# Kernel optimization log

Hardware: AMD Instinct MI355X
Metric: run time of the kernel (lower is better)

## Reference

```python
import jax, jax.numpy as jnp
import numpy as np

N_TOKEN = 50000
D_EMBED = 512
D_PROJ = 1024
CUTOFFS = [10000, 30000, 50000]  # cutoffs + [n_token]
N_CLUSTERS = len(CUTOFFS) - 1    # 2


def setup_inputs() -> dict:
    key = jax.random.key(0)
    ks = jax.random.split(key, 8)
    s = 0.02
    return {
        "hidden": jax.random.normal(ks[0], (4096, D_PROJ), jnp.float32),
        "target": jax.random.randint(ks[1], (4096,), 0, N_TOKEN, jnp.int64),
        # div_val == 1: one big output embedding, sliced per cluster
        "weight": jax.random.normal(ks[2], (N_TOKEN, D_EMBED), jnp.float32) * s,
        "bias": jnp.zeros((N_TOKEN,), jnp.float32),
        "cluster_weight": jax.random.normal(ks[3], (N_CLUSTERS, D_EMBED), jnp.float32) * s,
        "cluster_bias": jnp.zeros((N_CLUSTERS,), jnp.float32),
        # one [d_proj, d_embed] projection per cluster (head + 2 tails)
        "projs": jax.random.normal(ks[4], (N_CLUSTERS + 1, D_PROJ, D_EMBED), jnp.float32) * s,
    }


def _adaptive_logprob(hidden, target, weight, bias, cluster_weight, cluster_bias, projs):
    c0 = CUTOFFS[0]
    n = hidden.shape[0]
    # head: first-cluster vocab + one logit per tail cluster
    head_w = jnp.concatenate([weight[:c0], cluster_weight], axis=0)      # [c0+K, d_embed]
    head_b = jnp.concatenate([bias[:c0], cluster_bias], axis=0)          # [c0+K]
    h0 = hidden @ projs[0]                                               # [N, d_embed]
    head_lp = jax.nn.log_softmax(h0 @ head_w.T + head_b, axis=-1)        # [N, c0+K]

    # tokens in head cluster
    head_idx = jnp.clip(target, 0, c0 - 1)
    lp = jnp.take_along_axis(head_lp, head_idx[:, None], axis=1)[:, 0]
    out = jnp.where(target < c0, lp, 0.0)

    # tail clusters
    for i in range(1, N_CLUSTERS + 1):
        l, r = CUTOFFS[i - 1], CUTOFFS[i]
        hi = hidden @ projs[i]                                           # [N, d_embed]
        tail_lp = jax.nn.log_softmax(hi @ weight[l:r].T + bias[l:r], axis=-1)  # [N, r-l]
        t_idx = jnp.clip(target - l, 0, r - l - 1)
        tlp = jnp.take_along_axis(tail_lp, t_idx[:, None], axis=1)[:, 0]
        lp_i = head_lp[:, c0 + i - 1] + tlp
        out = jnp.where((target >= l) & (target < r), lp_i, out)

    return -out  # nll per token, [N]


def reference(hidden, target, weight, bias, cluster_weight, cluster_bias, projs):
    tgt_len = target.shape[0]
    nll = _adaptive_logprob(hidden[-tgt_len:], target, weight, bias,
                            cluster_weight, cluster_bias, projs)
    return nll.reshape(tgt_len, -1)  # [N, 1], matches loss.view(tgt_len, -1)
```

## Files before the change

kernel.cpp:

```cpp
#include <hip/hip_runtime.h>
#include <math.h>

#define NT 4096
#define DP 1024
#define DE 512
#define C0 10000
#define CUT1 30000
#define TAILV 20000
#define WROWS 50112
#define NBH 79
#define NBT 157

typedef unsigned short ushort_t;
typedef short bf8 __attribute__((ext_vector_type(8)));
typedef float f4 __attribute__((ext_vector_type(4)));

__device__ __forceinline__ ushort_t f2b(float f) {
    union { float f; unsigned int u; } v; v.f = f;
    unsigned int r = v.u + 0x7FFFu + ((v.u >> 16) & 1u);
    return (ushort_t)(r >> 16);
}
__device__ __forceinline__ float b2f(ushort_t u) {
    union { unsigned int u; float f; } v; v.u = ((unsigned int)u) << 16; return v.f;
}

__device__ __forceinline__ void gld16(const void* g, void* l) {
    __builtin_amdgcn_global_load_lds(
        (const __attribute__((address_space(1))) unsigned int*)g,
        (__attribute__((address_space(3))) unsigned int*)l, 16, 0, 0);
}

__device__ __forceinline__ int xcd_swz(int wgid, int nwg) {
    int q = nwg >> 3, r = nwg & 7;
    int xcd = wgid & 7, idx = wgid >> 3;
    int base = (xcd < r) ? xcd * (q + 1) : r * (q + 1) + (xcd - r) * q;
    return base + idx;
}

__global__ void cluster_kernel(const int* __restrict__ target,
                               int* __restrict__ cnt, int* __restrict__ list) {
    int t = blockIdx.x * blockDim.x + threadIdx.x;
    if (t >= NT) return;
    int tgt = target[t];
    int c = (tgt < C0) ? 0 : (tgt < CUT1 ? 1 : 2);
    if (c > 0) {
        int pos = atomicAdd(&cnt[c - 1], 1);
        list[(c - 1) * NT + pos] = t;
    }
}

__global__ __launch_bounds__(256)
void cast_pad(const float* __restrict__ in, ushort_t* __restrict__ out,
              int total4, int valid) {
    int i = blockIdx.x * 256 + threadIdx.x;
    if (i >= total4) return;
    int base = i * 4;
    unsigned long long p = 0ull;
    if (base < valid) {
        float4 v = *reinterpret_cast<const float4*>(in + base);
        p = (unsigned long long)f2b(v.x)
          | ((unsigned long long)f2b(v.y) << 16)
          | ((unsigned long long)f2b(v.z) << 32)
          | ((unsigned long long)f2b(v.w) << 48);
    }
    *reinterpret_cast<unsigned long long*>(out + base) = p;
}

__global__ __launch_bounds__(256)
void transpose_cast(const float* __restrict__ projs, ushort_t* __restrict__ out) {
    const int cblk = blockIdx.z;
    const int n0 = blockIdx.x * 32;
    const int k0 = blockIdx.y * 32;
    __shared__ float tile[32][33];
    const int tx = threadIdx.x & 31, ty = threadIdx.x >> 5;
    const float* src = projs + (size_t)cblk * DP * DE;
    #pragma unroll
    for (int j = 0; j < 4; ++j)
        tile[ty + j * 8][tx] = src[(size_t)(k0 + ty + j * 8) * DE + n0 + tx];
    __syncthreads();
    ushort_t* dst = out + (size_t)cblk * DE * DP;
    #pragma unroll
    for (int j = 0; j < 4; ++j)
        dst[(size_t)(n0 + ty + j * 8) * DP + k0 + tx] = f2b(tile[tx][ty + j * 8]);
}

template<int MODE>
__global__ __launch_bounds__(256, 4)
void gemm_bt(const ushort_t* __restrict__ Ab, const ushort_t* __restrict__ Bb,
             ushort_t* __restrict__ Cout, float* __restrict__ Sout,
             const float* __restrict__ bias,
             const int* __restrict__ cnt, const int* __restrict__ list,
             int K, int validN)
{
    const int tid = threadIdx.x;
    const int lane = tid & 63;
    const int wave = tid >> 6;
    const int wr = wave >> 1, wc = wave & 1;

    const int logical = xcd_swz(blockIdx.x, gridDim.x);
    const int bm = (logical & 31) * 128;
    const int bn = (logical >> 5) * 128;
    const int nb = logical >> 5;

    int n = 0;
    if (MODE == 0) {
        Bb += (size_t)blockIdx.z * DE * DP;
        Cout += (size_t)blockIdx.z * (size_t)NT * DE;
    }
    if (MODE == 2) {
        const int tail = blockIdx.z;
        n = cnt[tail];
        if (bm >= n) return;
        Ab += (size_t)(1 + tail) * NT * DE;
        Bb += (size_t)(C0 + tail * TAILV) * DE;
        bias += C0 + tail * TAILV;
        list += tail * NT;
        Sout += (size_t)tail * NBT * NT;
    }

    __shared__ __align__(16) unsigned char lds[32768];
    unsigned char* As = lds;
    unsigned char* Bs = lds + 16384;

    const int kswz = (lane & 7) ^ ((lane >> 3) & 7);
    const int kbase = kswz * 8;
    const int srow = wave * 8 + (lane >> 3);

    size_t arow[4], brow[4];
    #pragma unroll
    for (int s = 0; s < 4; ++s) {
        int lr = s * 32 + srow;
        int ga;
        if (MODE == 2) {
            int gr = bm + lr;
            ga = (gr < n) ? list[gr] : 0;
        } else ga = bm + lr;
        arow[s] = (size_t)ga * K;
        brow[s] = (size_t)(bn + lr) * K;
    }

    f4 acc[4][4];
    const f4 zero = {0.f, 0.f, 0.f, 0.f};
    #pragma unroll
    for (int i = 0; i < 4; ++i)
        #pragma unroll
        for (int j = 0; j < 4; ++j) acc[i][j] = zero;

    for (int kt = 0; kt < K; kt += 64) {
        if (kt) __syncthreads();
        #pragma unroll
        for (int s = 0; s < 4; ++s) {
            gld16(Ab + arow[s] + kt + kbase, As + s * 4096 + wave * 1024);
            gld16(Bb + brow[s] + kt + kbase, Bs + s * 4096 + wave * 1024);
        }
        __syncthreads();
        #pragma unroll
        for (int kh = 0; kh < 2; ++kh) {
            bf8 af[4], bv[4];
            #pragma unroll
            for (int i = 0; i < 4; ++i) {
                const int R = wr * 64 + i * 16 + (lane & 15);
                af[i] = *reinterpret_cast<const bf8*>(
                    As + R * 128 + (((kh * 4 + (lane >> 4)) ^ (R & 7)) << 4));
                const int Rb = wc * 64 + i * 16 + (lane & 15);
                bv[i] = *reinterpret_cast<const bf8*>(
                    Bs + Rb * 128 + (((kh * 4 + (lane >> 4)) ^ (Rb & 7)) << 4));
            }
            #pragma unroll
            for (int i = 0; i < 4; ++i)
                #pragma unroll
                for (int j = 0; j < 4; ++j)
                    acc[i][j] = __builtin_amdgcn_mfma_f32_16x16x32_bf16(
                        af[i], bv[j], acc[i][j], 0, 0, 0);
        }
    }

    if (MODE == 0) {
        #pragma unroll
        for (int i = 0; i < 4; ++i) {
            const int row = bm + wr * 64 + i * 16 + ((lane >> 4) << 2);
            #pragma unroll
            for (int j = 0; j < 4; ++j) {
                const int col = bn + wc * 64 + j * 16 + (lane & 15);
                #pragma unroll
                for (int r = 0; r < 4; ++r)
                    Cout[(size_t)(row + r) * DE + col] = f2b(acc[i][j][r]);
            }
        }
    } else {
        float rs[4][4];
        #pragma unroll
        for (int i = 0; i < 4; ++i)
            #pragma unroll
            for (int r = 0; r < 4; ++r) {
                float s = 0.f;
                #pragma unroll
                for (int j = 0; j < 4; ++j) {
                    const int col = bn + wc * 64 + j * 16 + (lane & 15);
                    if (col < validN) s += __expf(acc[i][j][r] + bias[col]);
                }
                rs[i][r] = s;
            }
        #pragma unroll
        for (int m = 1; m < 16; m <<= 1)
            #pragma unroll
            for (int i = 0; i < 4; ++i)
                #pragma unroll
                for (int r = 0; r < 4; ++r)
                    rs[i][r] += __shfl_xor(rs[i][r], m);
        float* ps = (float*)lds;
        __syncthreads();
        if ((lane & 15) == 0) {
            const int rb = (lane >> 4) << 2;
            #pragma unroll
            for (int i = 0; i < 4; ++i)
                #pragma unroll
                for (int r = 0; r < 4; ++r)
                    ps[wc * 128 + wr * 64 + i * 16 + rb + r] = rs[i][r];
        }
        __syncthreads();
        if (tid < 128) {
            float v = ps[tid] + ps[128 + tid];
            Sout[(size_t)nb * NT + bm + tid] = v;
        }
    }
}

__global__ __launch_bounds__(256)
void reduce_kernel(const float* __restrict__ Ph, const float* __restrict__ Pt,
                   const int* __restrict__ cnt, const int* __restrict__ list,
                   float* __restrict__ S_head, float* __restrict__ S_tail) {
    const int z = blockIdx.y;
    const int t = blockIdx.x * 256 + threadIdx.x;
    if (z == 0) {
        if (t >= NT) return;
        float s = 0.f;
        for (int nb = 0; nb < NBH; ++nb) s += Ph[(size_t)nb * NT + t];
        S_head[t] = s;
    } else {
        const int tail = z - 1;
        if (t >= cnt[tail]) return;
        const float* P = Pt + (size_t)tail * NBT * NT;
        float s = 0.f;
        for (int nb = 0; nb < NBT; ++nb) s += P[(size_t)nb * NT + t];
        S_tail[list[tail * NT + t]] = s;
    }
}

__global__ __launch_bounds__(64)
void finalize_kernel(const ushort_t* __restrict__ Hb, const int* __restrict__ target,
                     const float* __restrict__ weight, const float* __restrict__ bias,
                     const float* __restrict__ cw, const float* __restrict__ cb,
                     const float* __restrict__ S_head, const float* __restrict__ S_tail,
                     float* __restrict__ out)
{
    const int t = blockIdx.x, lane = threadIdx.x;
    const int tgt = target[t];
    const int c = (tgt < C0) ? 0 : (tgt < CUT1 ? 1 : 2);
    const int e = lane * 8;

    union { uint4 u; ushort_t s[8]; } h0;
    h0.u = *reinterpret_cast<const uint4*>(Hb + (size_t)t * DE + e);
    float hv[8];
    #pragma unroll
    for (int k = 0; k < 8; ++k) hv[k] = b2f(h0.s[k]);

    float c1 = 0.f, c2 = 0.f;
    #pragma unroll
    for (int k = 0; k < 8; ++k) {
        c1 += hv[k] * cw[e + k];
        c2 += hv[k] * cw[DE + e + k];
    }

    const ushort_t* hs = (c == 0) ? (Hb + (size_t)t * DE)
                                  : (Hb + ((size_t)c * NT + (size_t)t) * DE);
    union { uint4 u; ushort_t s[8]; } hc;
    hc.u = *reinterpret_cast<const uint4*>(hs + e);
    const float* wt = weight + (size_t)tgt * DE;
    float dt = 0.f;
    #pragma unroll
    for (int k = 0; k < 8; ++k) dt += b2f(hc.s[k]) * wt[e + k];

    #pragma unroll
    for (int m = 32; m; m >>= 1) {
        c1 += __shfl_xor(c1, m);
        c2 += __shfl_xor(c2, m);
        dt += __shfl_xor(dt, m);
    }
    if (lane == 0) {
        c1 += cb[0]; c2 += cb[1];
        const float S = S_head[t] + __expf(c1) + __expf(c2);
        const float lsh = logf(S);
        float res;
        if (c == 0) {
            res = lsh - (dt + bias[tgt]);
        } else {
            const float cl = (c == 1) ? c1 : c2;
            res = (lsh - cl) + (logf(S_tail[t]) - (dt + bias[tgt]));
        }
        out[t] = res;
    }
}

extern "C" void kernel_launch(void* const* d_in, const int* in_sizes, int n_in,
                              void* d_out, int out_size, void* d_ws, size_t ws_size,
                              hipStream_t stream) {
    const float* hidden = (const float*)d_in[0];
    const int*   target = (const int*)d_in[1];
    const float* weight = (const float*)d_in[2];
    const float* bias   = (const float*)d_in[3];
    const float* cw     = (const float*)d_in[4];
    const float* cb     = (const float*)d_in[5];
    const float* projs  = (const float*)d_in[6];
    float* out = (float*)d_out;

    char* w = (char*)d_ws;
    ushort_t* Hb      = (ushort_t*)w;  w += (size_t)3 * NT * DE * 2;
    ushort_t* hiddenb = (ushort_t*)w;  w += (size_t)NT * DP * 2;
    ushort_t* Wb      = (ushort_t*)w;  w += (size_t)WROWS * DE * 2;
    ushort_t* projsTb = (ushort_t*)w;  w += (size_t)3 * DE * DP * 2;
    float* S_head = (float*)w;         w += NT * 4;
    float* S_tail = (float*)w;         w += NT * 4;
    int* cnt      = (int*)w;           w += 32;
    int* list     = (int*)w;           w += 2 * NT * 4;
    float* Ph     = (float*)w;         w += (size_t)NBH * NT * 4;
    float* Pt     = (float*)w;         w += (size_t)2 * NBT * NT * 4;

    hipMemsetAsync(cnt, 0, 32, stream);
    cluster_kernel<<<NT / 256, 256, 0, stream>>>(target, cnt, list);
    cast_pad<<<(NT * DP / 4 + 255) / 256, 256, 0, stream>>>(
        hidden, hiddenb, NT * DP / 4, NT * DP);
    cast_pad<<<(WROWS * DE / 4 + 255) / 256, 256, 0, stream>>>(
        weight, Wb, WROWS * DE / 4, 50000 * DE);
    transpose_cast<<<dim3(DE / 32, DP / 32, 3), 256, 0, stream>>>(projs, projsTb);

    gemm_bt<0><<<dim3(32 * 4, 1, 3), 256, 0, stream>>>(
        hiddenb, projsTb, Hb, nullptr, nullptr, nullptr, nullptr, DP, DE);
    gemm_bt<1><<<dim3(32 * NBH, 1, 1), 256, 0, stream>>>(
        Hb, Wb, nullptr, Ph, bias, nullptr, nullptr, DE, C0);
    gemm_bt<2><<<dim3(32 * NBT, 1, 2), 256, 0, stream>>>(
        Hb, Wb, nullptr, Pt, bias, cnt, list, DE, TAILV);
    reduce_kernel<<<dim3(NT / 256, 3), 256, 0, stream>>>(
        Ph, Pt, cnt, list, S_head, S_tail);
    finalize_kernel<<<NT, 64, 0, stream>>>(
        Hb, target, weight, bias, cw, cb, S_head, S_tail, out);
}
```

Measured before the change: 298.8 us.

## Enlarge GEMM tiles to 256x256 with 8 waves and double-buffered LDS

The shared GEMM kernel moves from 128x128 tiles with 4 waves to 256x256 tiles with 8 waves. Each wave now computes a 128x64 sub-tile. Loads of the next K tile go into a second LDS buffer, so global-to-LDS transfer overlaps with the MFMA work on the current tile. This raises arithmetic intensity and hides load latency, at the cost of 128KB of LDS per block, lower occupancy, and fewer blocks. That risks under-filling the GPU for the small projection GEMM, where the grid is only 96 blocks.

```diff
diff --git a/kernel.cpp b/kernel.cpp
--- a/kernel.cpp
+++ b/kernel.cpp
@@ -7,9 +7,9 @@
 #define C0 10000
 #define CUT1 30000
 #define TAILV 20000
-#define WROWS 50112
-#define NBH 79
-#define NBT 157
+#define WROWS 50240
+#define NBH 40
+#define NBT 79
 
 typedef unsigned short ushort_t;
 typedef short bf8 __attribute__((ext_vector_type(8)));
@@ -85,7 +85,7 @@
 }
 
 template<int MODE>
-__global__ __launch_bounds__(256, 4)
+__global__ __launch_bounds__(512, 2)
 void gemm_bt(const ushort_t* __restrict__ Ab, const ushort_t* __restrict__ Bb,
              ushort_t* __restrict__ Cout, float* __restrict__ Sout,
              const float* __restrict__ bias,
@@ -94,13 +94,13 @@
 {
     const int tid = threadIdx.x;
     const int lane = tid & 63;
-    const int wave = tid >> 6;
-    const int wr = wave >> 1, wc = wave & 1;
+    const int w = tid >> 6;
+    const int wm = w >> 2, wn = w & 3;
 
     const int logical = xcd_swz(blockIdx.x, gridDim.x);
-    const int bm = (logical & 31) * 128;
-    const int bn = (logical >> 5) * 128;
-    const int nb = logical >> 5;
+    const int bm = (logical & 15) * 256;
+    const int bn = (logical >> 4) * 256;
+    const int nb = logical >> 4;
 
     int n = 0;
     if (MODE == 0) {
@@ -118,109 +118,119 @@
         Sout += (size_t)tail * NBT * NT;
     }
 
-    __shared__ __align__(16) unsigned char lds[32768];
-    unsigned char* As = lds;
-    unsigned char* Bs = lds + 16384;
-
-    const int kswz = (lane & 7) ^ ((lane >> 3) & 7);
-    const int kbase = kswz * 8;
-    const int srow = wave * 8 + (lane >> 3);
-
-    size_t arow[4], brow[4];
-    #pragma unroll
-    for (int s = 0; s < 4; ++s) {
-        int lr = s * 32 + srow;
+    __shared__ __align__(16) unsigned char lds[131072];
+
+    const int kswz = (lane & 7) ^ (lane >> 3);
+    const int dstoff = (w * 8 + (lane >> 3)) * 128 + (lane & 7) * 16;
+
+    const char* ap[4];
+    const char* bp[4];
+    #pragma unroll
+    for (int i = 0; i < 4; ++i) {
+        int r = i * 64 + w * 8 + (lane >> 3);
         int ga;
         if (MODE == 2) {
-            int gr = bm + lr;
+            int gr = bm + r;
             ga = (gr < n) ? list[gr] : 0;
-        } else ga = bm + lr;
-        arow[s] = (size_t)ga * K;
-        brow[s] = (size_t)(bn + lr) * K;
-    }
-
-    f4 acc[4][4];
+        } else ga = bm + r;
+        ap[i] = (const char*)Ab + (size_t)ga * K * 2 + kswz * 16;
+        bp[i] = (const char*)Bb + (size_t)(bn + r) * K * 2 + kswz * 16;
+    }
+
+    f4 acc[8][4];
     const f4 zero = {0.f, 0.f, 0.f, 0.f};
     #pragma unroll
-    for (int i = 0; i < 4; ++i)
+    for (int i = 0; i < 8; ++i)
         #pragma unroll
         for (int j = 0; j < 4; ++j) acc[i][j] = zero;
 
-    for (int kt = 0; kt < K; kt += 64) {
-        if (kt) __syncthreads();
-        #pragma unroll
-        for (int s = 0; s < 4; ++s) {
-            gld16(Ab + arow[s] + kt + kbase, As + s * 4096 + wave * 1024);
-            gld16(Bb + brow[s] + kt + kbase, Bs + s * 4096 + wave * 1024);
-        }
-        __syncthreads();
+    auto stage = [&](int t, unsigned char* buf) {
+        const int kb = t << 7;
+        #pragma unroll
+        for (int i = 0; i < 4; ++i) {
+            gld16(ap[i] + kb, buf + i * 8192 + dstoff);
+            gld16(bp[i] + kb, buf + 32768 + i * 8192 + dstoff);
+        }
+    };
+
+    const int ntiles = K >> 6;
+    stage(0, lds);
+    __syncthreads();
+
+    for (int t = 0; t < ntiles; ++t) {
+        unsigned char* cur = lds + ((t & 1) ? 65536 : 0);
+        if (t + 1 < ntiles)
+            stage(t + 1, lds + (((t + 1) & 1) ? 65536 : 0));
+        const unsigned char* As = cur;
+        const unsigned char* Bs = cur + 32768;
         #pragma unroll
         for (int kh = 0; kh < 2; ++kh) {
-            bf8 af[4], bv[4];
-            #pragma unroll
-            for (int i = 0; i < 4; ++i) {
-                const int R = wr * 64 + i * 16 + (lane & 15);
-                af[i] = *reinterpret_cast<const bf8*>(
-                    As + R * 128 + (((kh * 4 + (lane >> 4)) ^ (R & 7)) << 4));
-                const int Rb = wc * 64 + i * 16 + (lane & 15);
-                bv[i] = *reinterpret_cast<const bf8*>(
+            bf8 bv[4];
+            #pragma unroll
+            for (int nf = 0; nf < 4; ++nf) {
+                const int Rb = wn * 64 + nf * 16 + (lane & 15);
+                bv[nf] = *reinterpret_cast<const bf8*>(
                     Bs + Rb * 128 + (((kh * 4 + (lane >> 4)) ^ (Rb & 7)) << 4));
             }
             #pragma unroll
-            for (int i = 0; i < 4; ++i)
-                #pragma unroll
-                for (int j = 0; j < 4; ++j)
-                    acc[i][j] = __builtin_amdgcn_mfma_f32_16x16x32_bf16(
-                        af[i], bv[j], acc[i][j], 0, 0, 0);
-        }
+            for (int mf = 0; mf < 8; ++mf) {
+                const int Ra = wm * 128 + mf * 16 + (lane & 15);
+                bf8 af = *reinterpret_cast<const bf8*>(
+                    As + Ra * 128 + (((kh * 4 + (lane >> 4)) ^ (Ra & 7)) << 4));
+                #pragma unroll
+                for (int nf = 0; nf < 4; ++nf)
+                    acc[mf][nf] = __builtin_amdgcn_mfma_f32_16x16x32_bf16(
+                        af, bv[nf], acc[mf][nf], 0, 0, 0);
+            }
+        }
+        __syncthreads();
     }
 
     if (MODE == 0) {
         #pragma unroll
-        for (int i = 0; i < 4; ++i) {
-            const int row = bm + wr * 64 + i * 16 + ((lane >> 4) << 2);
-            #pragma unroll
-            for (int j = 0; j < 4; ++j) {
-                const int col = bn + wc * 64 + j * 16 + (lane & 15);
+        for (int mf = 0; mf < 8; ++mf) {
+            const int row = bm + wm * 128 + mf * 16 + ((lane >> 4) << 2);
+            #pragma unroll
+            for (int nf = 0; nf < 4; ++nf) {
+                const int col = bn + wn * 64 + nf * 16 + (lane & 15);
                 #pragma unroll
                 for (int r = 0; r < 4; ++r)
-                    Cout[(size_t)(row + r) * DE + col] = f2b(acc[i][j][r]);
+                    Cout[(size_t)(row + r) * DE + col] = f2b(acc[mf][nf][r]);
             }
         }
     } else {
-        float rs[4][4];
-        #pragma unroll
-        for (int i = 0; i < 4; ++i)
+        float rs[8][4];
+        #pragma unroll
+        for (int mf = 0; mf < 8; ++mf)
             #pragma unroll
             for (int r = 0; r < 4; ++r) {
                 float s = 0.f;
                 #pragma unroll
-                for (int j = 0; j < 4; ++j) {
-                    const int col = bn + wc * 64 + j * 16 + (lane & 15);
-                    if (col < validN) s += __expf(acc[i][j][r] + bias[col]);
+                for (int nf = 0; nf < 4; ++nf) {
+                    const int col = bn + wn * 64 + nf * 16 + (lane & 15);
+                    if (col < validN) s += __expf(acc[mf][nf][r] + bias[col]);
                 }
-                rs[i][r] = s;
+                rs[mf][r] = s;
             }
         #pragma unroll
         for (int m = 1; m < 16; m <<= 1)
             #pragma unroll
-            for (int i = 0; i < 4; ++i)
+            for (int mf = 0; mf < 8; ++mf)
                 #pragma unroll
                 for (int r = 0; r < 4; ++r)
-                    rs[i][r] += __shfl_xor(rs[i][r], m);
+                    rs[mf][r] += __shfl_xor(rs[mf][r], m);
         float* ps = (float*)lds;
-        __syncthreads();
         if ((lane & 15) == 0) {
             const int rb = (lane >> 4) << 2;
             #pragma unroll
-            for (int i = 0; i < 4; ++i)
+            for (int mf = 0; mf < 8; ++mf)
                 #pragma unroll
                 for (int r = 0; r < 4; ++r)
-                    ps[wc * 128 + wr * 64 + i * 16 + rb + r] = rs[i][r];
+                    ps[wn * 256 + wm * 128 + mf * 16 + rb + r] = rs[mf][r];
         }
         __syncthreads();
-        if (tid < 128) {
-            float v = ps[tid] + ps[128 + tid];
+        if (tid < 256) {
+            float v = ps[tid] + ps[256 + tid] + ps[512 + tid] + ps[768 + tid];
             Sout[(size_t)nb * NT + bm + tid] = v;
         }
     }
@@ -334,11 +344,11 @@
         weight, Wb, WROWS * DE / 4, 50000 * DE);
     transpose_cast<<<dim3(DE / 32, DP / 32, 3), 256, 0, stream>>>(projs, projsTb);
 
-    gemm_bt<0><<<dim3(32 * 4, 1, 3), 256, 0, stream>>>(
+    gemm_bt<0><<<dim3(16 * 2, 1, 3), 512, 0, stream>>>(
         hiddenb, projsTb, Hb, nullptr, nullptr, nullptr, nullptr, DP, DE);
-    gemm_bt<1><<<dim3(32 * NBH, 1, 1), 256, 0, stream>>>(
+    gemm_bt<1><<<dim3(16 * NBH, 1, 1), 512, 0, stream>>>(
         Hb, Wb, nullptr, Ph, bias, nullptr, nullptr, DE, C0);
-    gemm_bt<2><<<dim3(32 * NBT, 1, 2), 256, 0, stream>>>(
+    gemm_bt<2><<<dim3(16 * NBT, 1, 2), 512, 0, stream>>>(
         Hb, Wb, nullptr, Pt, bias, cnt, list, DE, TAILV);
     reduce_kernel<<<dim3(NT / 256, 3), 256, 0, stream>>>(
         Ph, Pt, cnt, list, S_head, S_tail);
```

Result: slower. 319.7 us (+7.0%).

## Merge head and tail logit GEMMs into one launch with staggered K start

Applied to the files above, without the earlier changes.

Merges the head-cluster and both tail-cluster sum-exp GEMMs into a single flat grid, so the tails' early-exited blocks no longer leave a separate launch with a thin tail wave. K becomes a template parameter so loops unroll at compile time. Each block starts its K loop at a different tile to spread concurrent loads across memory. Occupancy hint is raised from 4 to 5 blocks per CU, which may cost registers or cause spills.

```diff
diff --git a/kernel.cpp b/kernel.cpp
--- a/kernel.cpp
+++ b/kernel.cpp
@@ -84,39 +84,52 @@
         dst[(size_t)(n0 + ty + j * 8) * DP + k0 + tx] = f2b(tile[tx][ty + j * 8]);
 }
 
-template<int MODE>
-__global__ __launch_bounds__(256, 4)
-void gemm_bt(const ushort_t* __restrict__ Ab, const ushort_t* __restrict__ Bb,
-             ushort_t* __restrict__ Cout, float* __restrict__ Sout,
-             const float* __restrict__ bias,
-             const int* __restrict__ cnt, const int* __restrict__ list,
-             int K, int validN)
+template<int MODE, int KK>
+__global__ __launch_bounds__(256, 5)
+void gemm_bt(const ushort_t* __restrict__ A0, const ushort_t* __restrict__ B0,
+             ushort_t* __restrict__ Cout, float* __restrict__ Ph,
+             float* __restrict__ Pt, const float* __restrict__ bias,
+             const int* __restrict__ cnt, const int* __restrict__ list)
 {
+    constexpr int NTILES = KK >> 6;
     const int tid = threadIdx.x;
     const int lane = tid & 63;
     const int wave = tid >> 6;
     const int wr = wave >> 1, wc = wave & 1;
 
     const int logical = xcd_swz(blockIdx.x, gridDim.x);
-    const int bm = (logical & 31) * 128;
-    const int bn = (logical >> 5) * 128;
-    const int nb = logical >> 5;
-
-    int n = 0;
+    int mb, nbk, seg = 0, n = 0, validN = 0;
+    const ushort_t* Ab;
+    const ushort_t* Bb;
+    float* Sout = nullptr;
+    const float* bvec = nullptr;
+
     if (MODE == 0) {
-        Bb += (size_t)blockIdx.z * DE * DP;
+        mb = logical & 31; nbk = logical >> 5;
+        Ab = A0;
+        Bb = B0 + (size_t)blockIdx.z * DE * DP;
         Cout += (size_t)blockIdx.z * (size_t)NT * DE;
-    }
-    if (MODE == 2) {
-        const int tail = blockIdx.z;
-        n = cnt[tail];
-        if (bm >= n) return;
-        Ab += (size_t)(1 + tail) * NT * DE;
-        Bb += (size_t)(C0 + tail * TAILV) * DE;
-        bias += C0 + tail * TAILV;
-        list += tail * NT;
-        Sout += (size_t)tail * NBT * NT;
-    }
+    } else {
+        int l = logical;
+        if (l < 32 * NBH) {
+            seg = 0; mb = l & 31; nbk = l >> 5;
+            Ab = A0; Bb = B0; bvec = bias; validN = C0; Sout = Ph;
+        } else {
+            l -= 32 * NBH;
+            int z = (l < 32 * NBT) ? 0 : 1;
+            if (z) l -= 32 * NBT;
+            seg = 1 + z; mb = l & 31; nbk = l >> 5;
+            n = cnt[z];
+            if (mb * 128 >= n) return;
+            Ab = A0 + (size_t)(1 + z) * NT * DE;
+            Bb = B0 + (size_t)(C0 + z * TAILV) * DE;
+            bvec = bias + C0 + z * TAILV;
+            list += z * NT;
+            validN = TAILV;
+            Sout = Pt + (size_t)z * NBT * NT;
+        }
+    }
+    const int bm = mb * 128, bn = nbk * 128;
 
     __shared__ __align__(16) unsigned char lds[32768];
     unsigned char* As = lds;
@@ -131,12 +144,12 @@
     for (int s = 0; s < 4; ++s) {
         int lr = s * 32 + srow;
         int ga;
-        if (MODE == 2) {
+        if (MODE == 1 && seg > 0) {
             int gr = bm + lr;
             ga = (gr < n) ? list[gr] : 0;
         } else ga = bm + lr;
-        arow[s] = (size_t)ga * K;
-        brow[s] = (size_t)(bn + lr) * K;
+        arow[s] = (size_t)ga * KK;
+        brow[s] = (size_t)(bn + lr) * KK;
     }
 
     f4 acc[4][4];
@@ -146,11 +159,14 @@
         #pragma unroll
         for (int j = 0; j < 4; ++j) acc[i][j] = zero;
 
-    for (int kt = 0; kt < K; kt += 64) {
-        if (kt) __syncthreads();
+    const int start = (logical & 3) * (NTILES / 4);
+    for (int it = 0; it < NTILES; ++it) {
+        const int t = (it + start) & (NTILES - 1);
+        const int kt = t << 6;
+        if (it) __syncthreads();
         #pragma unroll
         for (int s = 0; s < 4; ++s) {
-            gld16(Ab + arow[s] + kt + kbase, As + s * 4096 + wave * 1024);
+            gld16(A0 + arow[s] + kt + kbase - (A0 - Ab), As + s * 4096 + wave * 1024);
             gld16(Bb + brow[s] + kt + kbase, Bs + s * 4096 + wave * 1024);
         }
         __syncthreads();
@@ -197,7 +213,7 @@
                 #pragma unroll
                 for (int j = 0; j < 4; ++j) {
                     const int col = bn + wc * 64 + j * 16 + (lane & 15);
-                    if (col < validN) s += __expf(acc[i][j][r] + bias[col]);
+                    if (col < validN) s += __expf(acc[i][j][r] + bvec[col]);
                 }
                 rs[i][r] = s;
             }
@@ -221,7 +237,7 @@
         __syncthreads();
         if (tid < 128) {
             float v = ps[tid] + ps[128 + tid];
-            Sout[(size_t)nb * NT + bm + tid] = v;
+            Sout[(size_t)nbk * NT + bm + tid] = v;
         }
     }
 }
@@ -334,12 +350,11 @@
         weight, Wb, WROWS * DE / 4, 50000 * DE);
     transpose_cast<<<dim3(DE / 32, DP / 32, 3), 256, 0, stream>>>(projs, projsTb);
 
-    gemm_bt<0><<<dim3(32 * 4, 1, 3), 256, 0, stream>>>(
-        hiddenb, projsTb, Hb, nullptr, nullptr, nullptr, nullptr, DP, DE);
-    gemm_bt<1><<<dim3(32 * NBH, 1, 1), 256, 0, stream>>>(
-        Hb, Wb, nullptr, Ph, bias, nullptr, nullptr, DE, C0);
-    gemm_bt<2><<<dim3(32 * NBT, 1, 2), 256, 0, stream>>>(
-        Hb, Wb, nullptr, Pt, bias, cnt, list, DE, TAILV);
+    gemm_bt<0, DP><<<dim3(32 * 4, 1, 3), 256, 0, stream>>>(
+        hiddenb, projsTb, Hb, nullptr, nullptr, nullptr, nullptr, nullptr);
+    gemm_bt<1, DE><<<dim3(32 * (NBH + 2 * NBT), 1, 1), 256, 0, stream>>>(
+        Hb, Wb, nullptr, Ph, Pt, bias, cnt, list);
+
     reduce_kernel<<<dim3(NT / 256, 3), 256, 0, stream>>>(
         Ph, Pt, cnt, list, S_head, S_tail);
     finalize_kernel<<<NT, 64, 0, stream>>>(
```

New measurement: 717.1 us. 2.4x slower.
